# Optimization experiments

Measured on AMD Instinct MI355X. Metric: run time of the kernel, lower is better.

The kernel has to match this reference:

```python
import jax, jax.numpy as jnp
import numpy as np

NUM_EMBEDDINGS = 1024
EMBEDDING_DIM = 64
COMMITMENT_COST = 0.25


def setup_inputs() -> dict:
    key = jax.random.key(0)
    k1, k2 = jax.random.split(key)
    z = jax.random.normal(k1, (32, EMBEDDING_DIM, 64, 64), dtype=jnp.float32)
    # nn.Embedding weight initialized uniform(-1/K, 1/K)
    lim = 1.0 / NUM_EMBEDDINGS
    codebook = jax.random.uniform(k2, (NUM_EMBEDDINGS, EMBEDDING_DIM),
                                  dtype=jnp.float32, minval=-lim, maxval=lim)
    return {"z": z, "codebook": codebook}


def reference(z, codebook):
    B, D, H, W = z.shape
    # (B, D, H, W) -> (B*H*W, D)
    z_flat = jnp.transpose(z, (0, 2, 3, 1)).reshape(-1, D)
    # squared L2 distances to all codebook entries: (N, K)
    distances = (jnp.sum(z_flat * z_flat, axis=1, keepdims=True)
                 + jnp.sum(codebook * codebook, axis=1)
                 - 2.0 * (z_flat @ codebook.T))
    encoding_indices = jnp.argmin(distances, axis=1)  # (N,)
    z_q = codebook[encoding_indices]                   # (N, D) gather
    z_q = jnp.transpose(z_q.reshape(B, H, W, D), (0, 3, 1, 2))
    vq_loss = jnp.mean((jax.lax.stop_gradient(z_q) - z) ** 2)
    commitment_loss = jnp.mean((z_q - jax.lax.stop_gradient(z)) ** 2)
    loss = vq_loss + COMMITMENT_COST * commitment_loss
    # straight-through estimator
    z_q_st = z + jax.lax.stop_gradient(z_q - z)
    return z_q_st, loss, encoding_indices.reshape(B, H * W)
```

## Files before the change

### kernel.cpp

```cpp
#include <hip/hip_runtime.h>

#define ZN 131072
#define DD 64
#define KK 1024
#define BSTRIDE 262144
#define DSTRIDE 4096
#define ZQ_ELEMS 8388608

#define WS_CSQ_OFF   16
#define WS_ZSQ_OFF   4112
#define WS_PACK_OFF  1052688
#define WS_CBB_OFF   2363408
#define WS_PAIR_OFF  2625552
#define PAIR_CAP     2097152u

typedef __attribute__((ext_vector_type(8))) short short8;
typedef __attribute__((ext_vector_type(4))) float f32x4;

__device__ __forceinline__ unsigned short f2bf_rne(float x) {
    unsigned u = __float_as_uint(x);
    return (unsigned short)((u + 0x7fffu + ((u >> 16) & 1u)) >> 16);
}

__device__ __forceinline__ float np_sumsq64(const float* a) {
    float r0 = __fmul_rn(a[0], a[0]), r1 = __fmul_rn(a[1], a[1]);
    float r2 = __fmul_rn(a[2], a[2]), r3 = __fmul_rn(a[3], a[3]);
    float r4 = __fmul_rn(a[4], a[4]), r5 = __fmul_rn(a[5], a[5]);
    float r6 = __fmul_rn(a[6], a[6]), r7 = __fmul_rn(a[7], a[7]);
#pragma unroll
    for (int i = 8; i < 64; i += 8) {
        r0 = __fadd_rn(r0, __fmul_rn(a[i + 0], a[i + 0]));
        r1 = __fadd_rn(r1, __fmul_rn(a[i + 1], a[i + 1]));
        r2 = __fadd_rn(r2, __fmul_rn(a[i + 2], a[i + 2]));
        r3 = __fadd_rn(r3, __fmul_rn(a[i + 3], a[i + 3]));
        r4 = __fadd_rn(r4, __fmul_rn(a[i + 4], a[i + 4]));
        r5 = __fadd_rn(r5, __fmul_rn(a[i + 5], a[i + 5]));
        r6 = __fadd_rn(r6, __fmul_rn(a[i + 6], a[i + 6]));
        r7 = __fadd_rn(r7, __fmul_rn(a[i + 7], a[i + 7]));
    }
    return __fadd_rn(__fadd_rn(__fadd_rn(r0, r1), __fadd_rn(r2, r3)),
                     __fadd_rn(__fadd_rn(r4, r5), __fadd_rn(r6, r7)));
}

__global__ __launch_bounds__(256) void vq_csq(const float* __restrict__ cb,
                                              float* __restrict__ csq) {
    int k = blockIdx.x * 256 + threadIdx.x;
    csq[k] = np_sumsq64(cb + k * DD);
}

__global__ __launch_bounds__(256) void vq_prep_b(const float* __restrict__ cb,
                                                 unsigned short* __restrict__ cbB) {
    int i = blockIdx.x * 256 + threadIdx.x;
    int k = i >> 6, d = i & 63;
    float c = cb[i];
    unsigned short hi = f2bf_rne(c);
    float hf = __uint_as_float((unsigned)hi << 16);
    unsigned short lo = f2bf_rne(c - hf);
    int ct = k >> 4, col = k & 15;
    int s = d >> 5, lg = (d >> 3) & 3, j = d & 7;
    int lane = col + 16 * lg;
    int base = ct * 2048 + s * 512 + lane * 8 + j;
    cbB[base] = hi;
    cbB[base + 1024] = lo;
}

__global__ __launch_bounds__(256) void vq_zsq(const float* __restrict__ z,
                                              float* __restrict__ zsq32) {
    int n = blockIdx.x * 256 + threadIdx.x;
    int b = n >> 12, p = n & 4095;
    const float* zp = z + (size_t)b * BSTRIDE + p;
    float r[8];
#pragma unroll
    for (int j = 0; j < 8; ++j) {
        float v = zp[(size_t)j * DSTRIDE];
        r[j] = __fmul_rn(v, v);
    }
#pragma unroll
    for (int i = 8; i < 64; i += 8)
#pragma unroll
        for (int j = 0; j < 8; ++j) {
            float v = zp[(size_t)(i + j) * DSTRIDE];
            r[j] = __fadd_rn(r[j], __fmul_rn(v, v));
        }
    zsq32[n] = __fadd_rn(__fadd_rn(__fadd_rn(r[0], r[1]), __fadd_rn(r[2], r[3])),
                         __fadd_rn(__fadd_rn(r[4], r[5]), __fadd_rn(r[6], r[7])));
}

__global__ __attribute__((amdgpu_waves_per_eu(2))) __launch_bounds__(256)
void vq_scan(const float* __restrict__ z,
             const unsigned short* __restrict__ cbB,
             const float* __restrict__ csq,
             float* __restrict__ idxf_out,
             unsigned* __restrict__ paircnt,
             unsigned* __restrict__ pairs,
             unsigned paircap) {
    __shared__ __align__(16) unsigned short aFrag[4][2][2][64][8];
    __shared__ float scsq[1024];
    __shared__ float smin1[4][64];
    __shared__ int sbest[4][64];
    __shared__ float gmin[64];
    __shared__ int ldsCnt[64];
    __shared__ unsigned candLDS[64][8];

    int t = threadIdx.x;
    int n0 = blockIdx.x * 64;
    int b = n0 >> 12, p0 = n0 & 4095;

    for (int i = t; i < 1024; i += 256) scsq[i] = csq[i];
    if (t < 64) ldsCnt[t] = 0;

    {
        int r = t & 63, gb = t >> 6;
        const float* zp = z + (size_t)b * BSTRIDE + p0 + r;
#pragma unroll
        for (int gg = 0; gg < 2; ++gg) {
            int g = (gb << 1) | gg;
            short8 hi8, lo8;
#pragma unroll
            for (int i2 = 0; i2 < 8; ++i2) {
                float v = zp[(size_t)(8 * g + i2) * DSTRIDE];
                unsigned short h = f2bf_rne(v);
                float hf = __uint_as_float((unsigned)h << 16);
                hi8[i2] = (short)h;
                lo8[i2] = (short)f2bf_rne(v - hf);
            }
            int rt = r >> 4, s = g >> 2, lane = (r & 15) + 16 * (g & 3);
            *(short8*)&aFrag[rt][s][0][lane][0] = hi8;
            *(short8*)&aFrag[rt][s][1][lane][0] = lo8;
        }
    }
    __syncthreads();

    int l = t & 63;
    int colcode = l & 15;

    short8 aH[4][2], aL[4][2];
#pragma unroll
    for (int rt = 0; rt < 4; ++rt)
#pragma unroll
        for (int s = 0; s < 2; ++s) {
            aH[rt][s] = *(const short8*)&aFrag[rt][s][0][l][0];
            aL[rt][s] = *(const short8*)&aFrag[rt][s][1][l][0];
        }

    int wv = __builtin_amdgcn_readfirstlane(t >> 6);

    float m1[4][4];
    int bst[4][4];
#pragma unroll
    for (int rt = 0; rt < 4; ++rt)
#pragma unroll
        for (int r = 0; r < 4; ++r) {
            m1[rt][r] = 3.4e38f;
            bst[rt][r] = 0;
        }

#pragma unroll 2
    for (int cti = 0; cti < 16; ++cti) {
        int ct = (wv << 4) + cti;
        const unsigned short* bp = cbB + ct * 2048 + (l << 3);
        short8 bh0 = *(const short8*)(bp);
        short8 bh1 = *(const short8*)(bp + 512);
        short8 bl0 = *(const short8*)(bp + 1024);
        short8 bl1 = *(const short8*)(bp + 1536);
        float cs = scsq[(ct << 4) + colcode];
        int code = (ct << 4) + colcode;
#pragma unroll
        for (int rt = 0; rt < 4; ++rt) {
            f32x4 acc = {0.f, 0.f, 0.f, 0.f};
            acc = __builtin_amdgcn_mfma_f32_16x16x32_bf16(aH[rt][0], bh0, acc, 0, 0, 0);
            acc = __builtin_amdgcn_mfma_f32_16x16x32_bf16(aH[rt][1], bh1, acc, 0, 0, 0);
            acc = __builtin_amdgcn_mfma_f32_16x16x32_bf16(aL[rt][0], bh0, acc, 0, 0, 0);
            acc = __builtin_amdgcn_mfma_f32_16x16x32_bf16(aL[rt][1], bh1, acc, 0, 0, 0);
            acc = __builtin_amdgcn_mfma_f32_16x16x32_bf16(aH[rt][0], bl0, acc, 0, 0, 0);
            acc = __builtin_amdgcn_mfma_f32_16x16x32_bf16(aH[rt][1], bl1, acc, 0, 0, 0);
#pragma unroll
            for (int r = 0; r < 4; ++r) {
                float dist = fmaf(-2.f, acc[r], cs);
                bool lt = dist < m1[rt][r];
                bst[rt][r] = lt ? code : bst[rt][r];
                m1[rt][r] = lt ? dist : m1[rt][r];
            }
        }
    }

#pragma unroll
    for (int m = 1; m <= 8; m <<= 1) {
#pragma unroll
        for (int rt = 0; rt < 4; ++rt)
#pragma unroll
            for (int r = 0; r < 4; ++r) {
                float o1 = __shfl_xor(m1[rt][r], m, 64);
                int ob = __shfl_xor(bst[rt][r], m, 64);
                bool take = (o1 < m1[rt][r]) ||
                            (o1 == m1[rt][r] && ob < bst[rt][r]);
                m1[rt][r] = take ? o1 : m1[rt][r];
                bst[rt][r] = take ? ob : bst[rt][r];
            }
    }

#pragma unroll
    for (int rt = 0; rt < 4; ++rt)
#pragma unroll
        for (int r = 0; r < 4; ++r)
            if ((l & 15) == r) {
                int row = (rt << 4) + ((l >> 4) << 2) + r;
                smin1[wv][row] = m1[rt][r];
                sbest[wv][row] = bst[rt][r];
            }
    __syncthreads();

    if (t < 64) {
        float g1 = smin1[0][t];
        int gb = sbest[0][t];
#pragma unroll
        for (int c = 1; c < 4; ++c) {
            float c1 = smin1[c][t];
            if (c1 < g1) {
                g1 = c1;
                gb = sbest[c][t];
            }
        }
        gmin[t] = g1;
        idxf_out[n0 + t] = (float)gb;
    }
    __syncthreads();

#pragma unroll 2
    for (int cti = 0; cti < 16; ++cti) {
        int ct = (wv << 4) + cti;
        const unsigned short* bp = cbB + ct * 2048 + (l << 3);
        short8 bh0 = *(const short8*)(bp);
        short8 bh1 = *(const short8*)(bp + 512);
        short8 bl0 = *(const short8*)(bp + 1024);
        short8 bl1 = *(const short8*)(bp + 1536);
        float cs = scsq[(ct << 4) + colcode];
        unsigned code = (unsigned)((ct << 4) + colcode);
#pragma unroll
        for (int rt = 0; rt < 4; ++rt) {
            f32x4 acc = {0.f, 0.f, 0.f, 0.f};
            acc = __builtin_amdgcn_mfma_f32_16x16x32_bf16(aH[rt][0], bh0, acc, 0, 0, 0);
            acc = __builtin_amdgcn_mfma_f32_16x16x32_bf16(aH[rt][1], bh1, acc, 0, 0, 0);
            acc = __builtin_amdgcn_mfma_f32_16x16x32_bf16(aL[rt][0], bh0, acc, 0, 0, 0);
            acc = __builtin_amdgcn_mfma_f32_16x16x32_bf16(aL[rt][1], bh1, acc, 0, 0, 0);
            acc = __builtin_amdgcn_mfma_f32_16x16x32_bf16(aH[rt][0], bl0, acc, 0, 0, 0);
            acc = __builtin_amdgcn_mfma_f32_16x16x32_bf16(aH[rt][1], bl1, acc, 0, 0, 0);
#pragma unroll
            for (int r = 0; r < 4; ++r) {
                float dist = fmaf(-2.f, acc[r], cs);
                int row = (rt << 4) + ((l >> 4) << 2) + r;
                if (dist < gmin[row] + 2e-4f) {
                    int pos = atomicAdd(&ldsCnt[row], 1);
                    if (pos < 8) candLDS[row][pos] = code;
                }
            }
        }
    }
    __syncthreads();

    if (t < 64) {
        int c = ldsCnt[t];
        int cc = (c > 8) ? 1024 : c;
        int run = cc;
#pragma unroll
        for (int off = 1; off < 64; off <<= 1) {
            int o = __shfl_up(run, off, 64);
            if (t >= off) run += o;
        }
        int total = __shfl(run, 63, 64);
        unsigned base = 0;
        if (t == 63) base = atomicAdd(paircnt, (unsigned)total);
        base = __shfl(base, 63, 64);
        unsigned start = base + (unsigned)(run - cc);
        unsigned nn = (unsigned)(n0 + t) << 10;
        if (c <= 8) {
            for (int i = 0; i < c; ++i)
                if (start + i < paircap) pairs[start + i] = nn | candLDS[t][i];
        } else {
            for (int i = 0; i < 1024; ++i)
                if (start + (unsigned)i < paircap) pairs[start + i] = nn | (unsigned)i;
        }
    }
}

__global__ __launch_bounds__(256) void vq_refine_pairs(
    const float* __restrict__ z,
    const float* __restrict__ cb,
    const float* __restrict__ csq,
    const float* __restrict__ zsq32,
    const unsigned* __restrict__ paircnt,
    const unsigned* __restrict__ pairs,
    unsigned paircap,
    unsigned long long* __restrict__ pack) {
    unsigned cnt = *paircnt;
    if (cnt > paircap) cnt = paircap;
    unsigned stride = gridDim.x * 256;
    for (unsigned i = blockIdx.x * 256 + threadIdx.x; i < cnt; i += stride) {
        unsigned pr = pairs[i];
        int n = (int)(pr >> 10);
        unsigned k = pr & 1023u;
        int b = n >> 12, p = n & 4095;
        const float* zp = z + (size_t)b * BSTRIDE + p;
        const float* cp = cb + k * DD;

        double a0 = 0.0, a1 = 0.0, a2 = 0.0, a3 = 0.0;
#pragma unroll
        for (int d = 0; d < DD; d += 4) {
            a0 = fma((double)zp[(size_t)(d + 0) * DSTRIDE], (double)cp[d + 0], a0);
            a1 = fma((double)zp[(size_t)(d + 1) * DSTRIDE], (double)cp[d + 1], a1);
            a2 = fma((double)zp[(size_t)(d + 2) * DSTRIDE], (double)cp[d + 2], a2);
            a3 = fma((double)zp[(size_t)(d + 3) * DSTRIDE], (double)cp[d + 3], a3);
        }
        double dot = (a0 + a1) + (a2 + a3);
        float twoC = (float)(2.0 * dot);
        float dist = __fsub_rn(__fadd_rn(zsq32[n], csq[k]), twoC);

        unsigned ub = __float_as_uint(dist);
        ub = (ub & 0x80000000u) ? ~ub : (ub | 0x80000000u);
        unsigned long long pk = ((unsigned long long)ub << 32) | k;
        atomicMin(&pack[n], pk);
    }
}

__global__ __launch_bounds__(256) void vq_gather_loss(const float* __restrict__ z,
                                                      const float* __restrict__ cb,
                                                      const unsigned long long* __restrict__ pack,
                                                      float* __restrict__ idxf,
                                                      float* __restrict__ zq_out,
                                                      double* __restrict__ acc) {
    int n = blockIdx.x * 256 + threadIdx.x;
    int b = n >> 12, p = n & 4095;
    const float* zp = z + (size_t)b * BSTRIDE + p;
    float* qp = zq_out + (size_t)b * BSTRIDE + p;

    unsigned long long pk = pack[n];
    int k;
    if (pk != 0xFFFFFFFFFFFFFFFFull) {
        k = (int)(unsigned)(pk & 0xFFFFFFFFull);
        idxf[n] = (float)k;
    } else {
        k = (int)idxf[n];
    }
    const float* c = cb + k * DD;

    float s = 0.f;
#pragma unroll
    for (int d = 0; d < DD; ++d) {
        float q = c[d];
        float diff = q - zp[(size_t)d * DSTRIDE];
        s = fmaf(diff, diff, s);
        qp[(size_t)d * DSTRIDE] = q;
    }

#pragma unroll
    for (int off = 32; off; off >>= 1) s += __shfl_down(s, off, 64);
    __shared__ float partial[4];
    if ((threadIdx.x & 63) == 0) partial[threadIdx.x >> 6] = s;
    __syncthreads();
    if (threadIdx.x == 0) {
        float t = (partial[0] + partial[1]) + (partial[2] + partial[3]);
        atomicAdd(acc, (double)t);
    }
}

__global__ void vq_finalize(const double* __restrict__ acc, float* __restrict__ loss_out) {
    *loss_out = (float)(1.25 * (*acc) / (double)ZQ_ELEMS);
}

extern "C" void kernel_launch(void* const* d_in, const int* in_sizes, int n_in,
                              void* d_out, int out_size, void* d_ws, size_t ws_size,
                              hipStream_t stream) {
    const float* z = (const float*)d_in[0];
    const float* cb = (const float*)d_in[1];
    float* out = (float*)d_out;

    float* zq_out = out;
    float* loss_out = out + ZQ_ELEMS;
    float* idxf_out = out + ZQ_ELEMS + 1;

    char* ws = (char*)d_ws;
    double* acc = (double*)ws;
    unsigned* paircnt = (unsigned*)(ws + 8);
    float* csq = (float*)(ws + WS_CSQ_OFF);
    float* zsq32 = (float*)(ws + WS_ZSQ_OFF);
    unsigned long long* pack = (unsigned long long*)(ws + WS_PACK_OFF);
    unsigned short* cbB = (unsigned short*)(ws + WS_CBB_OFF);
    unsigned* pairs = (unsigned*)(ws + WS_PAIR_OFF);

    unsigned paircap = 0;
    if (ws_size > WS_PAIR_OFF)
        paircap = (unsigned)((ws_size - WS_PAIR_OFF) / 4);
    if (paircap > PAIR_CAP) paircap = PAIR_CAP;

    hipMemsetAsync(d_ws, 0, 16, stream);
    hipMemsetAsync(ws + WS_PACK_OFF, 0xFF, ZN * 8, stream);

    vq_csq<<<KK / 256, 256, 0, stream>>>(cb, csq);
    vq_prep_b<<<KK * DD / 256, 256, 0, stream>>>(cb, cbB);
    vq_zsq<<<ZN / 256, 256, 0, stream>>>(z, zsq32);
    vq_scan<<<ZN / 64, 256, 0, stream>>>(z, cbB, csq, idxf_out, paircnt, pairs, paircap);
    vq_refine_pairs<<<2048, 256, 0, stream>>>(z, cb, csq, zsq32, paircnt, pairs, paircap, pack);
    vq_gather_loss<<<ZN / 256, 256, 0, stream>>>(z, cb, pack, idxf_out, zq_out, acc);
    vq_finalize<<<1, 1, 0, stream>>>(acc, loss_out);
}
```

Measured before the change: 260.2 us.

## Replace two-pass scan with single-pass threshold scan and overflow refine list

The scan kernel no longer makes two full passes over the codebook: one to find the exact minimum and a second to collect candidates. Instead it seeds a running minimum from a 64-code warmup and then collects candidates in a single pass, refreshing the threshold every 128 codes. Each wave now owns 16 rows and scans all 1024 codes, using two independent MFMA accumulators per tile for more instruction-level parallelism. Rows with more than 32 candidates, or that overflow the pair buffer, go to an overflow list that is refined exhaustively in fp64. Codebook prep is fused into one kernel, and the refine grid is halved. The running-minimum threshold admits more candidates early on, so refinement work may grow, and the warmup pass adds extra MFMA work per block.

```diff
diff --git a/kernel.cpp b/kernel.cpp
--- a/kernel.cpp
+++ b/kernel.cpp
@@ -9,10 +9,13 @@
 
 #define WS_CSQ_OFF   16
 #define WS_ZSQ_OFF   4112
+#define WS_OVF_OFF   528400
 #define WS_PACK_OFF  1052688
 #define WS_CBB_OFF   2363408
 #define WS_PAIR_OFF  2625552
 #define PAIR_CAP     2097152u
+
+#define RF_CAND 32
 
 typedef __attribute__((ext_vector_type(8))) short short8;
 typedef __attribute__((ext_vector_type(4))) float f32x4;
@@ -42,26 +45,25 @@
                      __fadd_rn(__fadd_rn(r4, r5), __fadd_rn(r6, r7)));
 }
 
-__global__ __launch_bounds__(256) void vq_csq(const float* __restrict__ cb,
-                                              float* __restrict__ csq) {
+__global__ __launch_bounds__(256) void vq_prep(const float* __restrict__ cb,
+                                               float* __restrict__ csq,
+                                               unsigned short* __restrict__ cbB) {
     int k = blockIdx.x * 256 + threadIdx.x;
-    csq[k] = np_sumsq64(cb + k * DD);
-}
-
-__global__ __launch_bounds__(256) void vq_prep_b(const float* __restrict__ cb,
-                                                 unsigned short* __restrict__ cbB) {
-    int i = blockIdx.x * 256 + threadIdx.x;
-    int k = i >> 6, d = i & 63;
-    float c = cb[i];
-    unsigned short hi = f2bf_rne(c);
-    float hf = __uint_as_float((unsigned)hi << 16);
-    unsigned short lo = f2bf_rne(c - hf);
+    const float* cp = cb + k * DD;
+    csq[k] = np_sumsq64(cp);
     int ct = k >> 4, col = k & 15;
-    int s = d >> 5, lg = (d >> 3) & 3, j = d & 7;
-    int lane = col + 16 * lg;
-    int base = ct * 2048 + s * 512 + lane * 8 + j;
-    cbB[base] = hi;
-    cbB[base + 1024] = lo;
+#pragma unroll
+    for (int d = 0; d < DD; ++d) {
+        float c = cp[d];
+        unsigned short hi = f2bf_rne(c);
+        float hf = __uint_as_float((unsigned)hi << 16);
+        unsigned short lo = f2bf_rne(c - hf);
+        int s = d >> 5, lg = (d >> 3) & 3, j = d & 7;
+        int lane = col + 16 * lg;
+        int base = ct * 2048 + s * 512 + lane * 8 + j;
+        cbB[base] = hi;
+        cbB[base + 1024] = lo;
+    }
 }
 
 __global__ __launch_bounds__(256) void vq_zsq(const float* __restrict__ z,
@@ -86,28 +88,34 @@
                          __fadd_rn(__fadd_rn(r[4], r[5]), __fadd_rn(r[6], r[7])));
 }
 
-__global__ __attribute__((amdgpu_waves_per_eu(2))) __launch_bounds__(256)
+#define MFMA_DIST(P, Q, A_H0, A_H1, A_L0, A_L1, B0, B1, B2, B3)               \
+    P = __builtin_amdgcn_mfma_f32_16x16x32_bf16(A_H0, B0, P, 0, 0, 0);        \
+    Q = __builtin_amdgcn_mfma_f32_16x16x32_bf16(A_H0, B2, Q, 0, 0, 0);        \
+    P = __builtin_amdgcn_mfma_f32_16x16x32_bf16(A_H1, B1, P, 0, 0, 0);        \
+    Q = __builtin_amdgcn_mfma_f32_16x16x32_bf16(A_H1, B3, Q, 0, 0, 0);        \
+    P = __builtin_amdgcn_mfma_f32_16x16x32_bf16(A_L0, B0, P, 0, 0, 0);        \
+    Q = __builtin_amdgcn_mfma_f32_16x16x32_bf16(A_L1, B1, Q, 0, 0, 0);
+
+__global__ __launch_bounds__(256)
 void vq_scan(const float* __restrict__ z,
              const unsigned short* __restrict__ cbB,
              const float* __restrict__ csq,
-             float* __restrict__ idxf_out,
              unsigned* __restrict__ paircnt,
+             unsigned* __restrict__ ovfcnt,
              unsigned* __restrict__ pairs,
+             int* __restrict__ ovflist,
              unsigned paircap) {
     __shared__ __align__(16) unsigned short aFrag[4][2][2][64][8];
     __shared__ float scsq[1024];
-    __shared__ float smin1[4][64];
-    __shared__ int sbest[4][64];
-    __shared__ float gmin[64];
-    __shared__ int ldsCnt[64];
-    __shared__ unsigned candLDS[64][8];
+    __shared__ int candCnt[64];
+    __shared__ unsigned short candK[64][RF_CAND];
 
     int t = threadIdx.x;
     int n0 = blockIdx.x * 64;
     int b = n0 >> 12, p0 = n0 & 4095;
 
     for (int i = t; i < 1024; i += 256) scsq[i] = csq[i];
-    if (t < 64) ldsCnt[t] = 0;
+    if (t < 64) candCnt[t] = 0;
 
     {
         int r = t & 63, gb = t >> 6;
@@ -133,125 +141,67 @@
 
     int l = t & 63;
     int colcode = l & 15;
-
-    short8 aH[4][2], aL[4][2];
-#pragma unroll
-    for (int rt = 0; rt < 4; ++rt)
-#pragma unroll
-        for (int s = 0; s < 2; ++s) {
-            aH[rt][s] = *(const short8*)&aFrag[rt][s][0][l][0];
-            aL[rt][s] = *(const short8*)&aFrag[rt][s][1][l][0];
-        }
-
-    int wv = __builtin_amdgcn_readfirstlane(t >> 6);
-
-    float m1[4][4];
-    int bst[4][4];
-#pragma unroll
-    for (int rt = 0; rt < 4; ++rt)
+    int w = __builtin_amdgcn_readfirstlane(t >> 6);
+
+    short8 aH0 = *(const short8*)&aFrag[w][0][0][l][0];
+    short8 aH1 = *(const short8*)&aFrag[w][1][0][l][0];
+    short8 aL0 = *(const short8*)&aFrag[w][0][1][l][0];
+    short8 aL1 = *(const short8*)&aFrag[w][1][1][l][0];
+
+    float m1[4];
+#pragma unroll
+    for (int r = 0; r < 4; ++r) m1[r] = 3.4e38f;
+
+    int rowb = (w << 4) + ((l >> 4) << 2);
+
+#pragma unroll
+    for (int pc = 0; pc < 4; ++pc) {
+        int ct = pc << 4;
+        const unsigned short* bp = cbB + ct * 2048 + (l << 3);
+        short8 b0 = *(const short8*)(bp);
+        short8 b1 = *(const short8*)(bp + 512);
+        short8 b2 = *(const short8*)(bp + 1024);
+        short8 b3 = *(const short8*)(bp + 1536);
+        float cs = scsq[(ct << 4) + colcode];
+        f32x4 p = {0.f, 0.f, 0.f, 0.f}, q = {0.f, 0.f, 0.f, 0.f};
+        MFMA_DIST(p, q, aH0, aH1, aL0, aL1, b0, b1, b2, b3)
+#pragma unroll
+        for (int r = 0; r < 4; ++r)
+            m1[r] = fminf(m1[r], fmaf(-2.f, p[r] + q[r], cs));
+    }
+
+    float thr[4];
+    for (int ph = 0; ph < 8; ++ph) {
+        __syncthreads();
 #pragma unroll
         for (int r = 0; r < 4; ++r) {
-            m1[rt][r] = 3.4e38f;
-            bst[rt][r] = 0;
-        }
-
+            float v = m1[r];
+            v = fminf(v, __shfl_xor(v, 1, 64));
+            v = fminf(v, __shfl_xor(v, 2, 64));
+            v = fminf(v, __shfl_xor(v, 4, 64));
+            v = fminf(v, __shfl_xor(v, 8, 64));
+            thr[r] = v + 2e-4f;
+        }
 #pragma unroll 2
-    for (int cti = 0; cti < 16; ++cti) {
-        int ct = (wv << 4) + cti;
-        const unsigned short* bp = cbB + ct * 2048 + (l << 3);
-        short8 bh0 = *(const short8*)(bp);
-        short8 bh1 = *(const short8*)(bp + 512);
-        short8 bl0 = *(const short8*)(bp + 1024);
-        short8 bl1 = *(const short8*)(bp + 1536);
-        float cs = scsq[(ct << 4) + colcode];
-        int code = (ct << 4) + colcode;
-#pragma unroll
-        for (int rt = 0; rt < 4; ++rt) {
-            f32x4 acc = {0.f, 0.f, 0.f, 0.f};
-            acc = __builtin_amdgcn_mfma_f32_16x16x32_bf16(aH[rt][0], bh0, acc, 0, 0, 0);
-            acc = __builtin_amdgcn_mfma_f32_16x16x32_bf16(aH[rt][1], bh1, acc, 0, 0, 0);
-            acc = __builtin_amdgcn_mfma_f32_16x16x32_bf16(aL[rt][0], bh0, acc, 0, 0, 0);
-            acc = __builtin_amdgcn_mfma_f32_16x16x32_bf16(aL[rt][1], bh1, acc, 0, 0, 0);
-            acc = __builtin_amdgcn_mfma_f32_16x16x32_bf16(aH[rt][0], bl0, acc, 0, 0, 0);
-            acc = __builtin_amdgcn_mfma_f32_16x16x32_bf16(aH[rt][1], bl1, acc, 0, 0, 0);
+        for (int c8 = 0; c8 < 8; ++c8) {
+            int ct = (ph << 3) | c8;
+            const unsigned short* bp = cbB + ct * 2048 + (l << 3);
+            short8 b0 = *(const short8*)(bp);
+            short8 b1 = *(const short8*)(bp + 512);
+            short8 b2 = *(const short8*)(bp + 1024);
+            short8 b3 = *(const short8*)(bp + 1536);
+            float cs = scsq[(ct << 4) + colcode];
+            unsigned code = (unsigned)((ct << 4) + colcode);
+            f32x4 p = {0.f, 0.f, 0.f, 0.f}, q = {0.f, 0.f, 0.f, 0.f};
+            MFMA_DIST(p, q, aH0, aH1, aL0, aL1, b0, b1, b2, b3)
 #pragma unroll
             for (int r = 0; r < 4; ++r) {
-                float dist = fmaf(-2.f, acc[r], cs);
-                bool lt = dist < m1[rt][r];
-                bst[rt][r] = lt ? code : bst[rt][r];
-                m1[rt][r] = lt ? dist : m1[rt][r];
-            }
-        }
-    }
-
-#pragma unroll
-    for (int m = 1; m <= 8; m <<= 1) {
-#pragma unroll
-        for (int rt = 0; rt < 4; ++rt)
-#pragma unroll
-            for (int r = 0; r < 4; ++r) {
-                float o1 = __shfl_xor(m1[rt][r], m, 64);
-                int ob = __shfl_xor(bst[rt][r], m, 64);
-                bool take = (o1 < m1[rt][r]) ||
-                            (o1 == m1[rt][r] && ob < bst[rt][r]);
-                m1[rt][r] = take ? o1 : m1[rt][r];
-                bst[rt][r] = take ? ob : bst[rt][r];
-            }
-    }
-
-#pragma unroll
-    for (int rt = 0; rt < 4; ++rt)
-#pragma unroll
-        for (int r = 0; r < 4; ++r)
-            if ((l & 15) == r) {
-                int row = (rt << 4) + ((l >> 4) << 2) + r;
-                smin1[wv][row] = m1[rt][r];
-                sbest[wv][row] = bst[rt][r];
-            }
-    __syncthreads();
-
-    if (t < 64) {
-        float g1 = smin1[0][t];
-        int gb = sbest[0][t];
-#pragma unroll
-        for (int c = 1; c < 4; ++c) {
-            float c1 = smin1[c][t];
-            if (c1 < g1) {
-                g1 = c1;
-                gb = sbest[c][t];
-            }
-        }
-        gmin[t] = g1;
-        idxf_out[n0 + t] = (float)gb;
-    }
-    __syncthreads();
-
-#pragma unroll 2
-    for (int cti = 0; cti < 16; ++cti) {
-        int ct = (wv << 4) + cti;
-        const unsigned short* bp = cbB + ct * 2048 + (l << 3);
-        short8 bh0 = *(const short8*)(bp);
-        short8 bh1 = *(const short8*)(bp + 512);
-        short8 bl0 = *(const short8*)(bp + 1024);
-        short8 bl1 = *(const short8*)(bp + 1536);
-        float cs = scsq[(ct << 4) + colcode];
-        unsigned code = (unsigned)((ct << 4) + colcode);
-#pragma unroll
-        for (int rt = 0; rt < 4; ++rt) {
-            f32x4 acc = {0.f, 0.f, 0.f, 0.f};
-            acc = __builtin_amdgcn_mfma_f32_16x16x32_bf16(aH[rt][0], bh0, acc, 0, 0, 0);
-            acc = __builtin_amdgcn_mfma_f32_16x16x32_bf16(aH[rt][1], bh1, acc, 0, 0, 0);
-            acc = __builtin_amdgcn_mfma_f32_16x16x32_bf16(aL[rt][0], bh0, acc, 0, 0, 0);
-            acc = __builtin_amdgcn_mfma_f32_16x16x32_bf16(aL[rt][1], bh1, acc, 0, 0, 0);
-            acc = __builtin_amdgcn_mfma_f32_16x16x32_bf16(aH[rt][0], bl0, acc, 0, 0, 0);
-            acc = __builtin_amdgcn_mfma_f32_16x16x32_bf16(aH[rt][1], bl1, acc, 0, 0, 0);
-#pragma unroll
-            for (int r = 0; r < 4; ++r) {
-                float dist = fmaf(-2.f, acc[r], cs);
-                int row = (rt << 4) + ((l >> 4) << 2) + r;
-                if (dist < gmin[row] + 2e-4f) {
-                    int pos = atomicAdd(&ldsCnt[row], 1);
-                    if (pos < 8) candLDS[row][pos] = code;
+                float dist = fmaf(-2.f, p[r] + q[r], cs);
+                m1[r] = fminf(m1[r], dist);
+                if (dist < thr[r]) {
+                    int row = rowb + r;
+                    int pos = atomicAdd(&candCnt[row], 1);
+                    if (pos < RF_CAND) candK[row][pos] = (unsigned short)code;
                 }
             }
         }
@@ -259,8 +209,9 @@
     __syncthreads();
 
     if (t < 64) {
-        int c = ldsCnt[t];
-        int cc = (c > 8) ? 1024 : c;
+        int c = candCnt[t];
+        bool ovf = (c > RF_CAND);
+        int cc = ovf ? 0 : c;
         int run = cc;
 #pragma unroll
         for (int off = 1; off < 64; off <<= 1) {
@@ -269,18 +220,45 @@
         }
         int total = __shfl(run, 63, 64);
         unsigned base = 0;
-        if (t == 63) base = atomicAdd(paircnt, (unsigned)total);
+        if (t == 63 && total) base = atomicAdd(paircnt, (unsigned)total);
         base = __shfl(base, 63, 64);
-        unsigned start = base + (unsigned)(run - cc);
-        unsigned nn = (unsigned)(n0 + t) << 10;
-        if (c <= 8) {
+        bool fits = (base <= paircap) && (base + (unsigned)total <= paircap);
+        bool toOvf = ovf || !fits;
+        unsigned long long mb = __ballot(toOvf);
+        int otot = __popcll(mb);
+        unsigned obase = 0;
+        if (t == 0 && otot) obase = atomicAdd(ovfcnt, (unsigned)otot);
+        obase = __shfl(obase, 0, 64);
+        if (toOvf) {
+            int opre = __popcll(mb & ((1ull << t) - 1ull));
+            ovflist[obase + opre] = n0 + t;
+        } else {
+            unsigned st = base + (unsigned)(run - cc);
+            unsigned nn = (unsigned)(n0 + t) << 10;
             for (int i = 0; i < c; ++i)
-                if (start + i < paircap) pairs[start + i] = nn | candLDS[t][i];
-        } else {
-            for (int i = 0; i < 1024; ++i)
-                if (start + (unsigned)i < paircap) pairs[start + i] = nn | (unsigned)i;
-        }
-    }
+                pairs[st + i] = nn | candK[t][i];
+        }
+    }
+}
+
+__device__ __forceinline__ unsigned long long ref_pack(const float* zp,
+                                                       const float* cp,
+                                                       float zsqn, float csqk,
+                                                       unsigned k) {
+    double a0 = 0.0, a1 = 0.0, a2 = 0.0, a3 = 0.0;
+#pragma unroll
+    for (int d = 0; d < DD; d += 4) {
+        a0 = fma((double)zp[(size_t)(d + 0) * DSTRIDE], (double)cp[d + 0], a0);
+        a1 = fma((double)zp[(size_t)(d + 1) * DSTRIDE], (double)cp[d + 1], a1);
+        a2 = fma((double)zp[(size_t)(d + 2) * DSTRIDE], (double)cp[d + 2], a2);
+        a3 = fma((double)zp[(size_t)(d + 3) * DSTRIDE], (double)cp[d + 3], a3);
+    }
+    double dot = (a0 + a1) + (a2 + a3);
+    float twoC = (float)(2.0 * dot);
+    float dist = __fsub_rn(__fadd_rn(zsqn, csqk), twoC);
+    unsigned ub = __float_as_uint(dist);
+    ub = (ub & 0x80000000u) ? ~ub : (ub | 0x80000000u);
+    return ((unsigned long long)ub << 32) | k;
 }
 
 __global__ __launch_bounds__(256) void vq_refine_pairs(
@@ -289,35 +267,37 @@
     const float* __restrict__ csq,
     const float* __restrict__ zsq32,
     const unsigned* __restrict__ paircnt,
+    const unsigned* __restrict__ ovfcnt,
     const unsigned* __restrict__ pairs,
+    const int* __restrict__ ovflist,
     unsigned paircap,
     unsigned long long* __restrict__ pack) {
+    unsigned stride = gridDim.x * 256;
+    unsigned tid = blockIdx.x * 256 + threadIdx.x;
+
     unsigned cnt = *paircnt;
     if (cnt > paircap) cnt = paircap;
-    unsigned stride = gridDim.x * 256;
-    for (unsigned i = blockIdx.x * 256 + threadIdx.x; i < cnt; i += stride) {
+    for (unsigned i = tid; i < cnt; i += stride) {
         unsigned pr = pairs[i];
-        int n = (int)(pr >> 10);
-        unsigned k = pr & 1023u;
+        unsigned n = pr >> 10;
+        if (n < (unsigned)ZN) {
+            unsigned k = pr & 1023u;
+            int b = n >> 12, p = n & 4095;
+            const float* zp = z + (size_t)b * BSTRIDE + p;
+            unsigned long long pk =
+                ref_pack(zp, cb + k * DD, zsq32[n], csq[k], k);
+            atomicMin(&pack[n], pk);
+        }
+    }
+
+    unsigned long long tot2 = (unsigned long long)(*ovfcnt) << 10;
+    for (unsigned long long wk = tid; wk < tot2; wk += stride) {
+        unsigned r = (unsigned)(wk >> 10);
+        unsigned k = (unsigned)(wk & 1023u);
+        int n = ovflist[r];
         int b = n >> 12, p = n & 4095;
         const float* zp = z + (size_t)b * BSTRIDE + p;
-        const float* cp = cb + k * DD;
-
-        double a0 = 0.0, a1 = 0.0, a2 = 0.0, a3 = 0.0;
-#pragma unroll
-        for (int d = 0; d < DD; d += 4) {
-            a0 = fma((double)zp[(size_t)(d + 0) * DSTRIDE], (double)cp[d + 0], a0);
-            a1 = fma((double)zp[(size_t)(d + 1) * DSTRIDE], (double)cp[d + 1], a1);
-            a2 = fma((double)zp[(size_t)(d + 2) * DSTRIDE], (double)cp[d + 2], a2);
-            a3 = fma((double)zp[(size_t)(d + 3) * DSTRIDE], (double)cp[d + 3], a3);
-        }
-        double dot = (a0 + a1) + (a2 + a3);
-        float twoC = (float)(2.0 * dot);
-        float dist = __fsub_rn(__fadd_rn(zsq32[n], csq[k]), twoC);
-
-        unsigned ub = __float_as_uint(dist);
-        ub = (ub & 0x80000000u) ? ~ub : (ub | 0x80000000u);
-        unsigned long long pk = ((unsigned long long)ub << 32) | k;
+        unsigned long long pk = ref_pack(zp, cb + k * DD, zsq32[n], csq[k], k);
         atomicMin(&pack[n], pk);
     }
 }
@@ -333,14 +313,8 @@
     const float* zp = z + (size_t)b * BSTRIDE + p;
     float* qp = zq_out + (size_t)b * BSTRIDE + p;
 
-    unsigned long long pk = pack[n];
-    int k;
-    if (pk != 0xFFFFFFFFFFFFFFFFull) {
-        k = (int)(unsigned)(pk & 0xFFFFFFFFull);
-        idxf[n] = (float)k;
-    } else {
-        k = (int)idxf[n];
-    }
+    int k = (int)(unsigned)(pack[n] & 1023ull);
+    idxf[n] = (float)k;
     const float* c = cb + k * DD;
 
     float s = 0.f;
@@ -381,8 +355,10 @@
     char* ws = (char*)d_ws;
     double* acc = (double*)ws;
     unsigned* paircnt = (unsigned*)(ws + 8);
+    unsigned* ovfcnt = (unsigned*)(ws + 12);
     float* csq = (float*)(ws + WS_CSQ_OFF);
     float* zsq32 = (float*)(ws + WS_ZSQ_OFF);
+    int* ovflist = (int*)(ws + WS_OVF_OFF);
     unsigned long long* pack = (unsigned long long*)(ws + WS_PACK_OFF);
     unsigned short* cbB = (unsigned short*)(ws + WS_CBB_OFF);
     unsigned* pairs = (unsigned*)(ws + WS_PAIR_OFF);
@@ -395,11 +371,12 @@
     hipMemsetAsync(d_ws, 0, 16, stream);
     hipMemsetAsync(ws + WS_PACK_OFF, 0xFF, ZN * 8, stream);
 
-    vq_csq<<<KK / 256, 256, 0, stream>>>(cb, csq);
-    vq_prep_b<<<KK * DD / 256, 256, 0, stream>>>(cb, cbB);
+    vq_prep<<<KK / 256, 256, 0, stream>>>(cb, csq, cbB);
     vq_zsq<<<ZN / 256, 256, 0, stream>>>(z, zsq32);
-    vq_scan<<<ZN / 64, 256, 0, stream>>>(z, cbB, csq, idxf_out, paircnt, pairs, paircap);
-    vq_refine_pairs<<<2048, 256, 0, stream>>>(z, cb, csq, zsq32, paircnt, pairs, paircap, pack);
+    vq_scan<<<ZN / 64, 256, 0, stream>>>(z, cbB, csq, paircnt, ovfcnt,
+                                         pairs, ovflist, paircap);
+    vq_refine_pairs<<<1024, 256, 0, stream>>>(z, cb, csq, zsq32, paircnt, ovfcnt,
+                                              pairs, ovflist, paircap, pack);
     vq_gather_loss<<<ZN / 256, 256, 0, stream>>>(z, cb, pack, idxf_out, zq_out, acc);
     vq_finalize<<<1, 1, 0, stream>>>(acc, loss_out);
 }
```

Result: slower. 285.2 us (+9.6%).
